# Kernel tuning notes

Measured on AMD Instinct MI355X. Metric: run time of the kernel, lower is better.

The kernel has to match this reference:

```python
import jax, jax.numpy as jnp
import numpy as np

N, E, HID, LAT = 50000, 800000, 128, 64
IN_NODE, IN_EDGE, NL = 11, 4, 2


def setup_inputs() -> dict:
    key = jax.random.key(0)
    ks = jax.random.split(key, 16)
    def rn(k, shape, scale=0.05):
        return jax.random.normal(k, shape, dtype=jnp.float32) * scale
    return {
        "h0": jax.random.normal(ks[0], (N, IN_NODE), jnp.float32),
        "label": jax.random.normal(ks[1], (N, 7), jnp.float32),
        "x": jax.random.normal(ks[2], (N, 3), jnp.float32),
        "edge_attr": jax.random.normal(ks[3], (E, IN_EDGE), jnp.float32),
        "eps": jax.random.normal(ks[4], (N, LAT), jnp.float32),
        "emb_w": rn(ks[5], (IN_NODE, HID)),
        "emb_b": jnp.zeros((HID,), jnp.float32),
        "edge_w1": rn(ks[6], (NL, 2 * HID + 1 + IN_EDGE, HID)),
        "edge_b1": jnp.zeros((NL, HID), jnp.float32),
        "edge_w2": rn(ks[7], (NL, HID, HID)),
        "edge_b2": jnp.zeros((NL, HID), jnp.float32),
        "node_w1": rn(ks[8], (NL, 3 * HID, HID)),
        "node_b1": jnp.zeros((NL, HID), jnp.float32),
        "node_w2": rn(ks[9], (NL, HID, HID)),
        "node_b2": jnp.zeros((NL, HID), jnp.float32),
        "mu_w": rn(ks[10], (HID + 7, LAT)),
        "mu_b": jnp.zeros((LAT,), jnp.float32),
        "var_w": rn(ks[11], (HID + 7, LAT)),
        "var_b": jnp.zeros((LAT,), jnp.float32),
        "edges": jax.random.randint(ks[12], (2, E), 0, N, dtype=jnp.int32),
        "n_nodes": N,
    }


def reference(h0, label, x, edge_attr, eps, emb_w, emb_b, edge_w1, edge_b1,
              edge_w2, edge_b2, node_w1, node_b1, node_w2, node_b2,
              mu_w, mu_b, var_w, var_b, edges, n_nodes):
    elu = jax.nn.elu
    row, col = edges[0], edges[1]
    # coord2radial: squared distance per edge [E,1]
    coord_diff = x[row] - x[col]
    radial = jnp.sum(coord_diff * coord_diff, axis=1, keepdims=True)
    # node embedding
    h = h0 @ emb_w + emb_b
    for i in range(NL):
        # edge_model: gather endpoints, fuse through 2-layer ELU MLP
        ef = jnp.concatenate([h[row], h[col], radial, edge_attr], axis=1)  # [E, 2H+1+IN_EDGE]
        ef = elu(ef @ edge_w1[i] + edge_b1[i])
        ef = elu(ef @ edge_w2[i] + edge_b2[i])
        # node_model: scatter-sum messages to source nodes, node_attr = h
        agg = jax.ops.segment_sum(ef, row, num_segments=n_nodes)  # [N, H]
        nf = jnp.concatenate([h, agg, h], axis=1)  # [N, 3H]
        nf = elu(nf @ node_w1[i] + node_b1[i])
        h = nf @ node_w2[i] + node_b2[i]  # recurrent=False: no residual
    hl = jnp.concatenate([h, label], axis=1)  # [N, H+7]
    mu = hl @ mu_w + mu_b
    log_var = hl @ var_w + var_b
    std = jnp.exp(log_var * 0.5)
    z = mu + 0.01 * eps * std
    return z
```

## Files before the change

### kernel.cpp

```cpp
#include <hip/hip_runtime.h>
#include <hip/hip_bf16.h>
#include <math.h>

#define N_NODES 50000
#define N_EDGES 800000
#define HID 128
#define LAT 64
#define IN_NODE 11
#define KN 256
#define KO 160
#define NST 264
#define TST 136
#define MST 132
#define HLST 168
#define OST 132
#define TE 32
#define NTPB 20
#define NTN 2
#define NSCAN 196
#define EB 3125
#define EMB_B 25000
#define WPB 32
#define ZB 100

typedef __attribute__((ext_vector_type(8))) short short8;
typedef __attribute__((ext_vector_type(4))) short short4v;
typedef __attribute__((ext_vector_type(4))) float floatx4;

__device__ __forceinline__ float elu_f(float v) { return v > 0.0f ? v : __expf(v) - 1.0f; }

__device__ __forceinline__ short f2bf(float f) {
    unsigned int u = __builtin_bit_cast(unsigned int, f);
    u += 0x7fffu + ((u >> 16) & 1u);
    return (short)(u >> 16);
}

__device__ __forceinline__ short2 f2bf2(float a, float b) {
    float2 p; p.x = a; p.y = b;
    __hip_bfloat162 h = __float22bfloat162_rn(p);
    short2 r;
    __builtin_memcpy(&r, &h, sizeof(r));
    return r;
}

__device__ __forceinline__ float bf2f(short s) {
    unsigned int u = ((unsigned int)(unsigned short)s) << 16;
    return __builtin_bit_cast(float, u);
}

__global__ void compose_k(const float* __restrict__ emb_w, const float* __restrict__ emb_b,
                          const float* __restrict__ ew1, float* __restrict__ cw) {
    int k0 = blockIdx.x;
    int mm = threadIdx.x;
    int m = mm & 127;
    int base = (mm < 128) ? 0 : 128;
    float s = 0.0f;
    for (int k = 0; k < 128; ++k) {
        float w = ew1[(size_t)(base + k) * 128 + m];
        float e = (k0 < 11) ? emb_w[k0 * 128 + k] : emb_b[k];
        s += e * w;
    }
    cw[k0 * 256 + mm] = s;
}

__global__ void prep_all(const int* __restrict__ edges, const float* __restrict__ h0,
                         const float* __restrict__ emb_w, const float* __restrict__ emb_b,
                         const float* __restrict__ ew1, const float* __restrict__ ew2,
                         const float* __restrict__ nw1, const float* __restrict__ nw2,
                         const float* __restrict__ mu_w, const float* __restrict__ mu_b,
                         const float* __restrict__ var_w, const float* __restrict__ var_b,
                         const float* __restrict__ cw,
                         int* __restrict__ cnt,
                         short* __restrict__ h_bf, float* __restrict__ aG,
                         short* __restrict__ ew2T,
                         short* __restrict__ nw1T, short* __restrict__ nw2T,
                         short* __restrict__ owT, short* __restrict__ awaT,
                         float* __restrict__ agg) {
    int b = blockIdx.x, t = threadIdx.x;
    if (b < EB) {
        int e = b * 256 + t;
        if (e >= N_EDGES) return;
        atomicAdd(&cnt[edges[e]], 1);
    } else if (b < EB + EMB_B) {
        int bb = b - EB;
        int n = bb * 2 + (t >> 7);
        int c = t & 127;
        if (n >= N_NODES) return;
        float h0v[IN_NODE];
        #pragma unroll
        for (int k = 0; k < IN_NODE; ++k) h0v[k] = h0[n*IN_NODE + k];
        float acc = emb_b[c];
        #pragma unroll
        for (int k = 0; k < IN_NODE; ++k) acc += h0v[k] * emb_w[k*HID + c];
        h_bf[(size_t)n*HID + c] = f2bf(acc);
        float s0 = cw[11*256 + c], s1 = cw[11*256 + 128 + c];
        #pragma unroll
        for (int k = 0; k < IN_NODE; ++k) {
            s0 += h0v[k] * cw[k*256 + c];
            s1 += h0v[k] * cw[k*256 + 128 + c];
        }
        aG[(size_t)n*256 + c]       = s0;
        aG[(size_t)n*256 + 128 + c] = s1;
    } else if (b < EB + EMB_B + WPB) {
        int idx = (b - EB - EMB_B) * 256 + t;
        int stride = WPB * 256;
        for (int i = idx; i < 2*128*128; i += stride) {
            int l = i / (128*128); int r = i % (128*128);
            int c = r / 128; int k = r % 128;
            ew2T[i] = f2bf(ew2[(size_t)l*128*128 + (size_t)k*128 + c]);
        }
        for (int i = idx; i < 2*128*KN; i += stride) {
            int l = i / (128*KN); int r = i % (128*KN);
            int c = r / KN; int k = r % KN;
            const float* base = nw1 + (size_t)l*384*128;
            float v = (k < 128) ? (base[(size_t)k*128 + c] + base[(size_t)(256+k)*128 + c])
                                : base[(size_t)k*128 + c];
            nw1T[i] = f2bf(v);
        }
        for (int i = idx; i < 2*128*128; i += stride) {
            int l = i / (128*128); int r = i % (128*128);
            int c = r / 128; int k = r % 128;
            nw2T[i] = f2bf(nw2[(size_t)l*128*128 + (size_t)k*128 + c]);
        }
        for (int i = idx; i < 128*KO; i += stride) {
            int c = i / KO; int k = i % KO;
            float v = 0.0f;
            if (c < 64) {
                if (k < 135) v = mu_w[(size_t)k*LAT + c];
                else if (k == 135) v = mu_b[c];
            } else {
                int cc = c - 64;
                if (k < 135) v = var_w[(size_t)k*LAT + cc];
                else if (k == 135) v = var_b[cc];
            }
            owT[i] = f2bf(v);
        }
        for (int i = idx; i < 2*256*128; i += stride) {
            int l = i / (256*128); int r = i % (256*128);
            int mm = r / 128; int k = r % 128;
            int kk = (mm < 128) ? k : 128 + k;
            awaT[i] = f2bf(ew1[(size_t)l*261*128 + (size_t)kk*128 + (mm & 127)]);
        }
    } else {
        int idx = (b - EB - EMB_B - WPB) * 256 + t;
        int stride = ZB * 256;
        float4 z = {0,0,0,0};
        float4* a4 = (float4*)agg;
        for (int i = idx; i < N_NODES*HID/4; i += stride) a4[i] = z;
    }
}

__global__ void scan_a(const int* __restrict__ cnt, int* __restrict__ cursor,
                       int* __restrict__ blk) {
    __shared__ int s[256];
    int b = blockIdx.x, t = threadIdx.x;
    int row = b * 256 + t;
    int v = (row < N_NODES) ? cnt[row] : 0;
    s[t] = v;
    __syncthreads();
    #pragma unroll
    for (int off = 1; off < 256; off <<= 1) {
        int add = (t >= off) ? s[t - off] : 0;
        __syncthreads();
        s[t] += add;
        __syncthreads();
    }
    if (row < N_NODES) cursor[row] = s[t] - v;
    if (t == 255) blk[b] = s[255];
}

__global__ void scan_b(int* __restrict__ blk) {
    __shared__ int s[256];
    int t = threadIdx.x;
    int v = (t < NSCAN) ? blk[t] : 0;
    s[t] = v;
    __syncthreads();
    #pragma unroll
    for (int off = 1; off < 256; off <<= 1) {
        int add = (t >= off) ? s[t - off] : 0;
        __syncthreads();
        s[t] += add;
        __syncthreads();
    }
    if (t < NSCAN) blk[t] = s[t] - v;
}

__global__ void csr_place(const int* __restrict__ edges, const float* __restrict__ x,
                          const float* __restrict__ edge_attr,
                          int* __restrict__ cursor, const int* __restrict__ blk,
                          int* __restrict__ srow, int* __restrict__ scol,
                          short* __restrict__ tail_s) {
    int e = blockIdx.x * 256 + threadIdx.x;
    if (e >= N_EDGES) return;
    int r = edges[e], c = edges[N_EDGES + e];
    float dx = x[r*3+0] - x[c*3+0];
    float dy = x[r*3+1] - x[c*3+1];
    float dz = x[r*3+2] - x[c*3+2];
    float radial = dx*dx + dy*dy + dz*dz;
    float4 ea = *(const float4*)(edge_attr + (size_t)e * 4);
    short8 s = { f2bf(radial), f2bf(ea.x), f2bf(ea.y), f2bf(ea.z), f2bf(ea.w), 0, 0, 0 };
    int pos = atomicAdd(&cursor[r], 1) + blk[r >> 8];
    srow[pos] = r; scol[pos] = c;
    *(short8*)(tail_s + (size_t)pos * 8) = s;
}

__global__ __launch_bounds__(256, 2) void edge_mfma_kernel(
    const float* __restrict__ aG, const short* __restrict__ tail_s,
    const int* __restrict__ srow, const int* __restrict__ scol,
    const float* __restrict__ w1c, const float* __restrict__ b1,
    const short* __restrict__ w2T, const float* __restrict__ b2,
    float* __restrict__ agg)
{
    __shared__ __align__(16) short t1[TE * TST];
    __shared__ __align__(16) float msgF[TE * MST];
    __shared__ int srowS[2][TE];
    int t = threadIdx.x;
    int lane = t & 63;
    int wv = t >> 6;
    int l15 = lane & 15;
    int quad = lane >> 4;
    int cg = t & 15;
    int elb = t >> 4;

    float w1cv[5][8];
    float b1v8[8];
    #pragma unroll
    for (int k = 0; k < 5; ++k)
        #pragma unroll
        for (int j = 0; j < 8; ++j)
            w1cv[k][j] = w1c[k*128 + cg*8 + j];
    #pragma unroll
    for (int j = 0; j < 8; ++j) b1v8[j] = b1[cg*8 + j];

    short8 aw2[2][4];
    float4 b2v[2];
    #pragma unroll
    for (int mi = 0; mi < 2; ++mi) {
        #pragma unroll
        for (int ks = 0; ks < 4; ++ks)
            aw2[mi][ks] = *(const short8*)&w2T[(size_t)(wv*32 + mi*16 + l15)*128 + ks*32 + quad*8];
        b2v[mi] = *(const float4*)&b2[wv*32 + mi*16 + quad*4];
    }

    for (int it = 0; it < NTPB; ++it) {
        int e0 = (blockIdx.x * NTPB + it) * TE;
        int pb = it & 1;
        if (t < TE) srowS[pb][t] = srow[e0 + t];

        #pragma unroll
        for (int ii = 0; ii < 2; ++ii) {
            int el = elb + ii*16;
            int e = e0 + el;
            int r = srow[e], c = scol[e];
            const float4* p1 = (const float4*)(aG + (size_t)r * 256 + cg*8);
            const float4* p2 = (const float4*)(aG + (size_t)c * 256 + 128 + cg*8);
            float4 x0 = p1[0], x1 = p1[1];
            float4 y0 = p2[0], y1 = p2[1];
            short8 tl = *(const short8*)(tail_s + (size_t)e * 8);
            float t0 = bf2f(tl[0]), t1f = bf2f(tl[1]), t2 = bf2f(tl[2]),
                  t3 = bf2f(tl[3]), t4 = bf2f(tl[4]);
            float s[8] = { x0.x+y0.x, x0.y+y0.y, x0.z+y0.z, x0.w+y0.w,
                           x1.x+y1.x, x1.y+y1.y, x1.z+y1.z, x1.w+y1.w };
            float v[8];
            #pragma unroll
            for (int j = 0; j < 8; ++j) {
                v[j] = elu_f(s[j] + b1v8[j]
                       + t0*w1cv[0][j] + t1f*w1cv[1][j] + t2*w1cv[2][j]
                       + t3*w1cv[3][j] + t4*w1cv[4][j]);
            }
            short2 q0 = f2bf2(v[0], v[1]), q1 = f2bf2(v[2], v[3]);
            short2 q2 = f2bf2(v[4], v[5]), q3 = f2bf2(v[6], v[7]);
            short8 o = { q0.x, q0.y, q1.x, q1.y, q2.x, q2.y, q3.x, q3.y };
            *(short8*)&t1[el*TST + cg*8] = o;
        }
        __syncthreads();

        floatx4 acc2[2][2] = {{{0,0,0,0},{0,0,0,0}},{{0,0,0,0},{0,0,0,0}}};
        #pragma unroll
        for (int ks = 0; ks < 4; ++ks) {
            int koff = ks*32 + quad*8;
            short8 bb0 = *(const short8*)&t1[l15*TST + koff];
            short8 bb1 = *(const short8*)&t1[(16 + l15)*TST + koff];
            acc2[0][0] = __builtin_amdgcn_mfma_f32_16x16x32_bf16(aw2[0][ks], bb0, acc2[0][0], 0, 0, 0);
            acc2[0][1] = __builtin_amdgcn_mfma_f32_16x16x32_bf16(aw2[0][ks], bb1, acc2[0][1], 0, 0, 0);
            acc2[1][0] = __builtin_amdgcn_mfma_f32_16x16x32_bf16(aw2[1][ks], bb0, acc2[1][0], 0, 0, 0);
            acc2[1][1] = __builtin_amdgcn_mfma_f32_16x16x32_bf16(aw2[1][ks], bb1, acc2[1][1], 0, 0, 0);
        }

        #pragma unroll
        for (int mi = 0; mi < 2; ++mi) {
            int cb = wv*32 + mi*16 + quad*4;
            #pragma unroll
            for (int ni = 0; ni < 2; ++ni) {
                float4 v = { elu_f(acc2[mi][ni][0] + b2v[mi].x), elu_f(acc2[mi][ni][1] + b2v[mi].y),
                             elu_f(acc2[mi][ni][2] + b2v[mi].z), elu_f(acc2[mi][ni][3] + b2v[mi].w) };
                *(float4*)&msgF[(ni*16 + l15)*MST + cb] = v;
            }
        }
        __syncthreads();

        {
            int ch = t & 127, half = t >> 7;
            int base = half * 16;
            int prow = srowS[pb][base];
            float run = 0.0f;
            #pragma unroll
            for (int i = 0; i < 16; ++i) {
                int rr = srowS[pb][base + i];
                if (rr != prow) {
                    unsafeAtomicAdd(&agg[(size_t)prow * HID + ch], run);
                    run = 0.0f; prow = rr;
                }
                run += msgF[(base + i)*MST + ch];
            }
            unsafeAtomicAdd(&agg[(size_t)prow * HID + ch], run);
        }
    }
}

__global__ __launch_bounds__(256, 2) void node_mfma_kernel(
    const short* __restrict__ h_bf, float* __restrict__ agg,
    const short* __restrict__ w1T, const float* __restrict__ b1,
    const short* __restrict__ w2T, const float* __restrict__ b2,
    const short* __restrict__ owT, const float* __restrict__ label,
    const float* __restrict__ eps, float* __restrict__ zout,
    short* __restrict__ hout_bf, const short* __restrict__ awaT1,
    float* __restrict__ aGout, int zero_agg, int do_out)
{
    __shared__ __align__(16) short featN[32 * NST];
    __shared__ __align__(16) short t1[32 * TST];
    __shared__ __align__(16) short hlB[32 * HLST];
    float* outB = (float*)featN;
    int t = threadIdx.x;
    int lane = t & 63;
    int wv = t >> 6;
    int l15 = lane & 15;
    int quad = lane >> 4;
    int nl = t >> 3, j = t & 7;

    short8 aw1[2][8], aw2[2][4];
    float4 b1v[2], b2v[2];
    #pragma unroll
    for (int mi = 0; mi < 2; ++mi) {
        #pragma unroll
        for (int ks = 0; ks < 8; ++ks)
            aw1[mi][ks] = *(const short8*)&w1T[(size_t)(wv*32 + mi*16 + l15)*KN + ks*32 + quad*8];
        #pragma unroll
        for (int ks = 0; ks < 4; ++ks)
            aw2[mi][ks] = *(const short8*)&w2T[(size_t)(wv*32 + mi*16 + l15)*128 + ks*32 + quad*8];
        b1v[mi] = *(const float4*)&b1[wv*32 + mi*16 + quad*4];
        b2v[mi] = *(const float4*)&b2[wv*32 + mi*16 + quad*4];
    }

    for (int it = 0; it < NTN; ++it) {
        int n0 = (blockIdx.x * NTN + it) * 32;
        if (n0 >= N_NODES) break;
        __syncthreads();

        int n = n0 + nl;
        int idx = n < N_NODES ? n : N_NODES - 1;
        {
            const short8* hp = (const short8*)(h_bf + (size_t)idx * HID + j*16);
            short8 s0 = hp[0], s1 = hp[1];
            const float4* ap = (const float4*)(agg + (size_t)idx * HID) + j*4;
            float4 u0 = ap[0], u1 = ap[1], u2 = ap[2], u3 = ap[3];
            short2 p0 = f2bf2(u0.x, u0.y), p1 = f2bf2(u0.z, u0.w);
            short2 p2 = f2bf2(u1.x, u1.y), p3 = f2bf2(u1.z, u1.w);
            short2 p4 = f2bf2(u2.x, u2.y), p5 = f2bf2(u2.z, u2.w);
            short2 p6 = f2bf2(u3.x, u3.y), p7 = f2bf2(u3.z, u3.w);
            short8 s2 = { p0.x, p0.y, p1.x, p1.y, p2.x, p2.y, p3.x, p3.y };
            short8 s3 = { p4.x, p4.y, p5.x, p5.y, p6.x, p6.y, p7.x, p7.y };
            *(short8*)&featN[nl*NST + j*16]       = s0;
            *(short8*)&featN[nl*NST + j*16 + 8]   = s1;
            *(short8*)&featN[nl*NST + 128 + j*16]     = s2;
            *(short8*)&featN[nl*NST + 128 + j*16 + 8] = s3;
        }
        __syncthreads();

        if (zero_agg && n < N_NODES) {
            float4 z = {0,0,0,0};
            float4* ap = (float4*)(agg + (size_t)n * HID) + j*4;
            ap[0] = z; ap[1] = z; ap[2] = z; ap[3] = z;
        }

        floatx4 acc[2][2] = {{{0,0,0,0},{0,0,0,0}},{{0,0,0,0},{0,0,0,0}}};
        #pragma unroll
        for (int ks = 0; ks < 8; ++ks) {
            int koff = ks*32 + quad*8;
            short8 bb0 = *(const short8*)&featN[l15*NST + koff];
            short8 bb1 = *(const short8*)&featN[(16 + l15)*NST + koff];
            acc[0][0] = __builtin_amdgcn_mfma_f32_16x16x32_bf16(aw1[0][ks], bb0, acc[0][0], 0, 0, 0);
            acc[0][1] = __builtin_amdgcn_mfma_f32_16x16x32_bf16(aw1[0][ks], bb1, acc[0][1], 0, 0, 0);
            acc[1][0] = __builtin_amdgcn_mfma_f32_16x16x32_bf16(aw1[1][ks], bb0, acc[1][0], 0, 0, 0);
            acc[1][1] = __builtin_amdgcn_mfma_f32_16x16x32_bf16(aw1[1][ks], bb1, acc[1][1], 0, 0, 0);
        }

        #pragma unroll
        for (int mi = 0; mi < 2; ++mi) {
            int cb = wv*32 + mi*16 + quad*4;
            #pragma unroll
            for (int ni = 0; ni < 2; ++ni) {
                short2 p0 = f2bf2(elu_f(acc[mi][ni][0] + b1v[mi].x),
                                  elu_f(acc[mi][ni][1] + b1v[mi].y));
                short2 p1 = f2bf2(elu_f(acc[mi][ni][2] + b1v[mi].z),
                                  elu_f(acc[mi][ni][3] + b1v[mi].w));
                short4v s = { p0.x, p0.y, p1.x, p1.y };
                *(short4v*)&t1[(ni*16 + l15)*TST + cb] = s;
            }
        }
        __syncthreads();

        floatx4 acc2[2][2] = {{{0,0,0,0},{0,0,0,0}},{{0,0,0,0},{0,0,0,0}}};
        #pragma unroll
        for (int ks = 0; ks < 4; ++ks) {
            int koff = ks*32 + quad*8;
            short8 bb0 = *(const short8*)&t1[l15*TST + koff];
            short8 bb1 = *(const short8*)&t1[(16 + l15)*TST + koff];
            acc2[0][0] = __builtin_amdgcn_mfma_f32_16x16x32_bf16(aw2[0][ks], bb0, acc2[0][0], 0, 0, 0);
            acc2[0][1] = __builtin_amdgcn_mfma_f32_16x16x32_bf16(aw2[0][ks], bb1, acc2[0][1], 0, 0, 0);
            acc2[1][0] = __builtin_amdgcn_mfma_f32_16x16x32_bf16(aw2[1][ks], bb0, acc2[1][0], 0, 0, 0);
            acc2[1][1] = __builtin_amdgcn_mfma_f32_16x16x32_bf16(aw2[1][ks], bb1, acc2[1][1], 0, 0, 0);
        }

        if (!do_out) {
            __syncthreads();
            #pragma unroll
            for (int mi = 0; mi < 2; ++mi) {
                int cb = wv*32 + mi*16 + quad*4;
                #pragma unroll
                for (int ni = 0; ni < 2; ++ni) {
                    int nn = n0 + ni*16 + l15;
                    short2 p0 = f2bf2(acc2[mi][ni][0] + b2v[mi].x, acc2[mi][ni][1] + b2v[mi].y);
                    short2 p1 = f2bf2(acc2[mi][ni][2] + b2v[mi].z, acc2[mi][ni][3] + b2v[mi].w);
                    short4v s = { p0.x, p0.y, p1.x, p1.y };
                    if (nn < N_NODES) *(short4v*)&hout_bf[(size_t)nn*HID + cb] = s;
                    *(short4v*)&t1[(ni*16 + l15)*TST + cb] = s;
                }
            }
            __syncthreads();
            floatx4 accA[4][2] = {{{0,0,0,0},{0,0,0,0}},{{0,0,0,0},{0,0,0,0}},
                                  {{0,0,0,0},{0,0,0,0}},{{0,0,0,0},{0,0,0,0}}};
            #pragma unroll
            for (int ks = 0; ks < 4; ++ks) {
                int koff = ks*32 + quad*8;
                short8 bb0 = *(const short8*)&t1[l15*TST + koff];
                short8 bb1 = *(const short8*)&t1[(16 + l15)*TST + koff];
                #pragma unroll
                for (int mi = 0; mi < 4; ++mi) {
                    short8 wf = *(const short8*)&awaT1[(size_t)(wv*64 + mi*16 + l15)*128 + ks*32 + quad*8];
                    accA[mi][0] = __builtin_amdgcn_mfma_f32_16x16x32_bf16(wf, bb0, accA[mi][0], 0, 0, 0);
                    accA[mi][1] = __builtin_amdgcn_mfma_f32_16x16x32_bf16(wf, bb1, accA[mi][1], 0, 0, 0);
                }
            }
            #pragma unroll
            for (int mi = 0; mi < 4; ++mi) {
                int mm = wv*64 + mi*16 + quad*4;
                #pragma unroll
                for (int ni = 0; ni < 2; ++ni) {
                    int nn = n0 + ni*16 + l15;
                    if (nn < N_NODES) {
                        float4 v = { accA[mi][ni][0], accA[mi][ni][1], accA[mi][ni][2], accA[mi][ni][3] };
                        *(float4*)&aGout[(size_t)nn*256 + mm] = v;
                    }
                }
            }
        } else {
            #pragma unroll
            for (int mi = 0; mi < 2; ++mi) {
                int cb = wv*32 + mi*16 + quad*4;
                #pragma unroll
                for (int ni = 0; ni < 2; ++ni) {
                    short2 p0 = f2bf2(acc2[mi][ni][0] + b2v[mi].x, acc2[mi][ni][1] + b2v[mi].y);
                    short2 p1 = f2bf2(acc2[mi][ni][2] + b2v[mi].z, acc2[mi][ni][3] + b2v[mi].w);
                    short4v s = { p0.x, p0.y, p1.x, p1.y };
                    *(short4v*)&hlB[(ni*16 + l15)*HLST + cb] = s;
                }
            }
            if (t < 32) {
                int nn = n0 + t;
                int ii = nn < N_NODES ? nn : N_NODES - 1;
                const float* lp = label + (size_t)ii * 7;
                short8 s = { f2bf(lp[0]), f2bf(lp[1]), f2bf(lp[2]), f2bf(lp[3]),
                             f2bf(lp[4]), f2bf(lp[5]), f2bf(lp[6]), f2bf(1.0f) };
                short8 z = {0,0,0,0,0,0,0,0};
                *(short8*)&hlB[t*HLST + 128] = s;
                *(short8*)&hlB[t*HLST + 136] = z;
                *(short8*)&hlB[t*HLST + 144] = z;
                *(short8*)&hlB[t*HLST + 152] = z;
            }
            __syncthreads();

            floatx4 accO[2][2] = {{{0,0,0,0},{0,0,0,0}},{{0,0,0,0},{0,0,0,0}}};
            short8 awO[2][5];
            #pragma unroll
            for (int mi = 0; mi < 2; ++mi)
                #pragma unroll
                for (int ks = 0; ks < 5; ++ks)
                    awO[mi][ks] = *(const short8*)&owT[(size_t)(wv*32 + mi*16 + l15)*KO + ks*32 + quad*8];
            #pragma unroll
            for (int ks = 0; ks < 5; ++ks) {
                int koff = ks*32 + quad*8;
                short8 bb0 = *(const short8*)&hlB[l15*HLST + koff];
                short8 bb1 = *(const short8*)&hlB[(16 + l15)*HLST + koff];
                accO[0][0] = __builtin_amdgcn_mfma_f32_16x16x32_bf16(awO[0][ks], bb0, accO[0][0], 0, 0, 0);
                accO[0][1] = __builtin_amdgcn_mfma_f32_16x16x32_bf16(awO[0][ks], bb1, accO[0][1], 0, 0, 0);
                accO[1][0] = __builtin_amdgcn_mfma_f32_16x16x32_bf16(awO[1][ks], bb0, accO[1][0], 0, 0, 0);
                accO[1][1] = __builtin_amdgcn_mfma_f32_16x16x32_bf16(awO[1][ks], bb1, accO[1][1], 0, 0, 0);
            }
            #pragma unroll
            for (int mi = 0; mi < 2; ++mi) {
                int cg2 = wv*32 + mi*16 + quad*4;
                #pragma unroll
                for (int ni = 0; ni < 2; ++ni) {
                    float4 v = { accO[mi][ni][0], accO[mi][ni][1], accO[mi][ni][2], accO[mi][ni][3] };
                    *(float4*)&outB[(ni*16 + l15)*OST + cg2] = v;
                }
            }
            __syncthreads();

            {
                int c = t & 63, g = t >> 6;
                #pragma unroll
                for (int i = 0; i < 8; ++i) {
                    int nloc = g*8 + i;
                    int nn = n0 + nloc;
                    if (nn < N_NODES) {
                        float mu = outB[nloc*OST + c];
                        float va = outB[nloc*OST + 64 + c];
                        zout[(size_t)nn*LAT + c] = mu + 0.01f * eps[(size_t)nn*LAT + c] * __expf(va * 0.5f);
                    }
                }
            }
        }
    }
}

extern "C" void kernel_launch(void* const* d_in, const int* in_sizes, int n_in,
                              void* d_out, int out_size, void* d_ws, size_t ws_size,
                              hipStream_t stream) {
    const float* h0        = (const float*)d_in[0];
    const float* label     = (const float*)d_in[1];
    const float* x         = (const float*)d_in[2];
    const float* edge_attr = (const float*)d_in[3];
    const float* eps       = (const float*)d_in[4];
    const float* emb_w     = (const float*)d_in[5];
    const float* emb_b     = (const float*)d_in[6];
    const float* edge_w1   = (const float*)d_in[7];
    const float* edge_b1   = (const float*)d_in[8];
    const float* edge_w2   = (const float*)d_in[9];
    const float* edge_b2   = (const float*)d_in[10];
    const float* node_w1   = (const float*)d_in[11];
    const float* node_b1   = (const float*)d_in[12];
    const float* node_w2   = (const float*)d_in[13];
    const float* node_b2   = (const float*)d_in[14];
    const float* mu_w      = (const float*)d_in[15];
    const float* mu_b      = (const float*)d_in[16];
    const float* var_w     = (const float*)d_in[17];
    const float* var_b     = (const float*)d_in[18];
    const int*   edges     = (const int*)d_in[19];
    float* out = (float*)d_out;

    float* agg      = (float*)d_ws;
    float* aG       = agg + (size_t)N_NODES * HID;
    short* h_bf     = (short*)(aG + (size_t)N_NODES * 256);
    short* tail_s   = h_bf + (size_t)N_NODES * HID;
    int*   cnt      = (int*)(tail_s + (size_t)N_EDGES * 8);
    int*   cursor   = cnt + N_NODES;
    int*   blk      = cursor + N_NODES;
    int*   srow     = blk + 256;
    int*   scol     = srow + N_EDGES;
    short* ew2T     = (short*)(scol + N_EDGES);
    short* nw1T     = ew2T + 2*128*128;
    short* nw2T     = nw1T + 2*128*KN;
    short* owT      = nw2T + 2*128*128;
    short* awaT     = owT + 128*KO;
    float* cw       = (float*)(awaT + 2*256*128);

    hipMemsetAsync(cnt, 0, N_NODES * sizeof(int), stream);
    compose_k<<<12, 256, 0, stream>>>(emb_w, emb_b, edge_w1, cw);
    prep_all<<<EB + EMB_B + WPB + ZB, 256, 0, stream>>>(
        edges, h0, emb_w, emb_b,
        edge_w1, edge_w2, node_w1, node_w2,
        mu_w, mu_b, var_w, var_b, cw,
        cnt, h_bf, aG, ew2T, nw1T, nw2T, owT, awaT, agg);
    scan_a<<<NSCAN, 256, 0, stream>>>(cnt, cursor, blk);
    scan_b<<<1, 256, 0, stream>>>(blk);
    csr_place<<<(N_EDGES + 255) / 256, 256, 0, stream>>>(edges, x, edge_attr, cursor, blk,
                                                         srow, scol, tail_s);

    for (int l = 0; l < 2; ++l) {
        edge_mfma_kernel<<<N_EDGES / TE / NTPB, 256, 0, stream>>>(
            aG, tail_s, srow, scol,
            edge_w1 + (size_t)l * 261 * 128 + 256 * 128, edge_b1 + l * HID,
            ew2T + (size_t)l * 128 * 128, edge_b2 + l * HID, agg);
        node_mfma_kernel<<<(N_NODES/32 + NTN) / NTN, 256, 0, stream>>>(
            h_bf, agg,
            nw1T + (size_t)l * 128 * KN, node_b1 + l * HID,
            nw2T + (size_t)l * 128 * 128, node_b2 + l * HID,
            owT, label, eps, out, h_bf,
            awaT + 256 * 128, aG,
            (l == 0) ? 1 : 0, (l == 1) ? 1 : 0);
    }
}
```

Before: 592.4 us.

## Store gathered node projections in bf16 and prefetch next edge tile

The per-node first-layer edge projections (aG) are now stored as bf16 instead of fp32, which halves the bytes gathered per edge endpoint in the edge kernel. The edge kernel also software-pipelines its loads, prefetching the next tile's gathered rows and tail features into registers while the current tile's MFMA work runs. The __syncthreads calls are replaced with an LDS-only wait plus barrier. The costs are lost precision in the pre-activation sums and higher register pressure from the prefetch buffers.

```diff
diff --git a/kernel.cpp b/kernel.cpp
--- a/kernel.cpp
+++ b/kernel.cpp
@@ -48,6 +48,12 @@
     return __builtin_bit_cast(float, u);
 }
 
+__device__ __forceinline__ void lds_barrier() {
+    asm volatile("s_waitcnt lgkmcnt(0)" ::: "memory");
+    __builtin_amdgcn_s_barrier();
+    asm volatile("" ::: "memory");
+}
+
 __global__ void compose_k(const float* __restrict__ emb_w, const float* __restrict__ emb_b,
                           const float* __restrict__ ew1, float* __restrict__ cw) {
     int k0 = blockIdx.x;
@@ -71,7 +77,7 @@
                          const float* __restrict__ var_w, const float* __restrict__ var_b,
                          const float* __restrict__ cw,
                          int* __restrict__ cnt,
-                         short* __restrict__ h_bf, float* __restrict__ aG,
+                         short* __restrict__ h_bf, short* __restrict__ aGb,
                          short* __restrict__ ew2T,
                          short* __restrict__ nw1T, short* __restrict__ nw2T,
                          short* __restrict__ owT, short* __restrict__ awaT,
@@ -99,8 +105,8 @@
             s0 += h0v[k] * cw[k*256 + c];
             s1 += h0v[k] * cw[k*256 + 128 + c];
         }
-        aG[(size_t)n*256 + c]       = s0;
-        aG[(size_t)n*256 + 128 + c] = s1;
+        aGb[(size_t)n*256 + c]       = f2bf(s0);
+        aGb[(size_t)n*256 + 128 + c] = f2bf(s1);
     } else if (b < EB + EMB_B + WPB) {
         int idx = (b - EB - EMB_B) * 256 + t;
         int stride = WPB * 256;
@@ -205,7 +211,7 @@
 }
 
 __global__ __launch_bounds__(256, 2) void edge_mfma_kernel(
-    const float* __restrict__ aG, const short* __restrict__ tail_s,
+    const short* __restrict__ aGb, const short* __restrict__ tail_s,
     const int* __restrict__ srow, const int* __restrict__ scol,
     const float* __restrict__ w1c, const float* __restrict__ b1,
     const short* __restrict__ w2T, const float* __restrict__ b2,
@@ -242,6 +248,21 @@
         b2v[mi] = *(const float4*)&b2[wv*32 + mi*16 + quad*4];
     }
 
+    short8 pa1[2], pa2[2], ptl[2];
+    auto prefetch = [&](int s_) {
+        int e0 = (blockIdx.x * NTPB + s_) * TE;
+        #pragma unroll
+        for (int ii = 0; ii < 2; ++ii) {
+            int e = e0 + elb + ii*16;
+            e = e < N_EDGES ? e : N_EDGES - 1;
+            int r = srow[e], c = scol[e];
+            pa1[ii] = *(const short8*)(aGb + (size_t)r * 256 + cg*8);
+            pa2[ii] = *(const short8*)(aGb + (size_t)c * 256 + 128 + cg*8);
+            ptl[ii] = *(const short8*)(tail_s + (size_t)e * 8);
+        }
+    };
+    prefetch(0);
+
     for (int it = 0; it < NTPB; ++it) {
         int e0 = (blockIdx.x * NTPB + it) * TE;
         int pb = it & 1;
@@ -250,21 +271,14 @@
         #pragma unroll
         for (int ii = 0; ii < 2; ++ii) {
             int el = elb + ii*16;
-            int e = e0 + el;
-            int r = srow[e], c = scol[e];
-            const float4* p1 = (const float4*)(aG + (size_t)r * 256 + cg*8);
-            const float4* p2 = (const float4*)(aG + (size_t)c * 256 + 128 + cg*8);
-            float4 x0 = p1[0], x1 = p1[1];
-            float4 y0 = p2[0], y1 = p2[1];
-            short8 tl = *(const short8*)(tail_s + (size_t)e * 8);
-            float t0 = bf2f(tl[0]), t1f = bf2f(tl[1]), t2 = bf2f(tl[2]),
-                  t3 = bf2f(tl[3]), t4 = bf2f(tl[4]);
-            float s[8] = { x0.x+y0.x, x0.y+y0.y, x0.z+y0.z, x0.w+y0.w,
-                           x1.x+y1.x, x1.y+y1.y, x1.z+y1.z, x1.w+y1.w };
+            short8 A = pa1[ii], B = pa2[ii], T = ptl[ii];
+            float t0 = bf2f(T[0]), t1f = bf2f(T[1]), t2 = bf2f(T[2]),
+                  t3 = bf2f(T[3]), t4 = bf2f(T[4]);
             float v[8];
             #pragma unroll
             for (int j = 0; j < 8; ++j) {
-                v[j] = elu_f(s[j] + b1v8[j]
+                float s = bf2f(A[j]) + bf2f(B[j]);
+                v[j] = elu_f(s + b1v8[j]
                        + t0*w1cv[0][j] + t1f*w1cv[1][j] + t2*w1cv[2][j]
                        + t3*w1cv[3][j] + t4*w1cv[4][j]);
             }
@@ -273,7 +287,9 @@
             short8 o = { q0.x, q0.y, q1.x, q1.y, q2.x, q2.y, q3.x, q3.y };
             *(short8*)&t1[el*TST + cg*8] = o;
         }
-        __syncthreads();
+        if (it + 1 < NTPB) prefetch(it + 1);
+
+        lds_barrier();
 
         floatx4 acc2[2][2] = {{{0,0,0,0},{0,0,0,0}},{{0,0,0,0},{0,0,0,0}}};
         #pragma unroll
@@ -297,7 +313,7 @@
                 *(float4*)&msgF[(ni*16 + l15)*MST + cb] = v;
             }
         }
-        __syncthreads();
+        lds_barrier();
 
         {
             int ch = t & 127, half = t >> 7;
@@ -325,7 +341,7 @@
     const short* __restrict__ owT, const float* __restrict__ label,
     const float* __restrict__ eps, float* __restrict__ zout,
     short* __restrict__ hout_bf, const short* __restrict__ awaT1,
-    float* __restrict__ aGout, int zero_agg, int do_out)
+    short* __restrict__ aGbout, int zero_agg, int do_out)
 {
     __shared__ __align__(16) short featN[32 * NST];
     __shared__ __align__(16) short t1[32 * TST];
@@ -459,8 +475,10 @@
                 for (int ni = 0; ni < 2; ++ni) {
                     int nn = n0 + ni*16 + l15;
                     if (nn < N_NODES) {
-                        float4 v = { accA[mi][ni][0], accA[mi][ni][1], accA[mi][ni][2], accA[mi][ni][3] };
-                        *(float4*)&aGout[(size_t)nn*256 + mm] = v;
+                        short2 p0 = f2bf2(accA[mi][ni][0], accA[mi][ni][1]);
+                        short2 p1 = f2bf2(accA[mi][ni][2], accA[mi][ni][3]);
+                        short4v s = { p0.x, p0.y, p1.x, p1.y };
+                        *(short4v*)&aGbout[(size_t)nn*256 + mm] = s;
                     }
                 }
             }
@@ -561,8 +579,8 @@
     float* out = (float*)d_out;
 
     float* agg      = (float*)d_ws;
-    float* aG       = agg + (size_t)N_NODES * HID;
-    short* h_bf     = (short*)(aG + (size_t)N_NODES * 256);
+    short* aGb      = (short*)(agg + (size_t)N_NODES * HID);
+    short* h_bf     = aGb + (size_t)N_NODES * 256;
     short* tail_s   = h_bf + (size_t)N_NODES * HID;
     int*   cnt      = (int*)(tail_s + (size_t)N_EDGES * 8);
     int*   cursor   = cnt + N_NODES;
@@ -582,7 +600,7 @@
         edges, h0, emb_w, emb_b,
         edge_w1, edge_w2, node_w1, node_w2,
         mu_w, mu_b, var_w, var_b, cw,
-        cnt, h_bf, aG, ew2T, nw1T, nw2T, owT, awaT, agg);
+        cnt, h_bf, aGb, ew2T, nw1T, nw2T, owT, awaT, agg);
     scan_a<<<NSCAN, 256, 0, stream>>>(cnt, cursor, blk);
     scan_b<<<1, 256, 0, stream>>>(blk);
     csr_place<<<(N_EDGES + 255) / 256, 256, 0, stream>>>(edges, x, edge_attr, cursor, blk,
@@ -590,7 +608,7 @@
 
     for (int l = 0; l < 2; ++l) {
         edge_mfma_kernel<<<N_EDGES / TE / NTPB, 256, 0, stream>>>(
-            aG, tail_s, srow, scol,
+            aGb, tail_s, srow, scol,
             edge_w1 + (size_t)l * 261 * 128 + 256 * 128, edge_b1 + l * HID,
             ew2T + (size_t)l * 128 * 128, edge_b2 + l * HID, agg);
         node_mfma_kernel<<<(N_NODES/32 + NTN) / NTN, 256, 0, stream>>>(
@@ -598,7 +616,7 @@
             nw1T + (size_t)l * 128 * KN, node_b1 + l * HID,
             nw2T + (size_t)l * 128 * 128, node_b2 + l * HID,
             owT, label, eps, out, h_bf,
-            awaT + 256 * 128, aG,
+            awaT + 256 * 128, aGb,
             (l == 0) ? 1 : 0, (l == 1) ? 1 : 0);
     }
 }
```

Measured after the change: 571.3 us. 1.04x faster.
